# Kernel tuning notes

Hardware: AMD Instinct MI355X
Metric: run time of the kernel (lower is better)

Reference implementation:

```python
import jax, jax.numpy as jnp
import numpy as np

B, LQ, LKV = 4, 2048, 2048
E, AUG, H = 2048, 1024, 16
DH = E // H
EPS = 1e-6


def setup_inputs() -> dict:
    key = jax.random.key(0)
    ks = jax.random.split(key, 6)
    s = lambda d: 1.0 / np.sqrt(d)
    return {
        "query": jax.random.normal(ks[0], (B, LQ, E), jnp.float32),
        "aug_hidden_state": jax.random.normal(ks[1], (B, LKV, AUG), jnp.float32),
        "aug_mask": jnp.ones((B, LKV), jnp.float32),
        "proj_w": jax.random.normal(ks[2], (E, AUG), jnp.float32) * s(AUG),
        "proj_b": jnp.zeros((E,), jnp.float32),
        "in_proj_w": jax.random.normal(ks[3], (3 * E, E), jnp.float32) * s(E),
        "in_proj_b": jnp.zeros((3 * E,), jnp.float32),
        "out_proj_w": jax.random.normal(ks[4], (E, E), jnp.float32) * s(E),
        "out_proj_b": jnp.zeros((E,), jnp.float32),
        "rms_w": jnp.zeros((E,), jnp.float32),
    }


def reference(query, aug_hidden_state, aug_mask, proj_w, proj_b,
              in_proj_w, in_proj_b, out_proj_w, out_proj_b, rms_w):
    del aug_mask  # asserted but never used by the original forward
    # key and value: two identical Linear calls in the original -> same tensor
    kv = aug_hidden_state @ proj_w.T + proj_b                      # [B,LKV,E]
    wq, wk, wv = jnp.split(in_proj_w, 3, axis=0)
    bq, bk, bv = jnp.split(in_proj_b, 3, axis=0)
    q = (query @ wq.T + bq).reshape(B, LQ, H, DH)
    k = (kv @ wk.T + bk).reshape(B, LKV, H, DH)
    v = (kv @ wv.T + bv).reshape(B, LKV, H, DH)
    scale = 1.0 / np.sqrt(DH)
    scores = jnp.einsum("bqhd,bkhd->bhqk", q * scale, k)           # [B,H,LQ,LKV]
    attn = jax.nn.softmax(scores, axis=-1)
    ctx = jnp.einsum("bhqk,bkhd->bqhd", attn, v).reshape(B, LQ, E)
    attn_out = ctx @ out_proj_w.T + out_proj_b                      # [B,LQ,E]
    # GemmaRMSNorm: fp32 norm, (1 + weight) gain
    x32 = attn_out.astype(jnp.float32)
    normed = x32 * jax.lax.rsqrt(jnp.mean(x32 * x32, axis=-1, keepdims=True) + EPS)
    attn_out = (normed * (1.0 + rms_w)).astype(attn_out.dtype)
    return attn_out + query
```

## Files before the change

### kernel.cpp

```cpp
#include <hip/hip_runtime.h>
#include <hip/hip_bf16.h>
#include <stdint.h>

#define B_   4
#define LQ_  2048
#define LKV_ 2048
#define E_   2048
#define AUG_ 1024
#define H_   16
#define DH_  128

typedef unsigned short u16;
typedef __bf16 bf16x8 __attribute__((ext_vector_type(8)));
typedef float f32x4 __attribute__((ext_vector_type(4)));
typedef float f32x16 __attribute__((ext_vector_type(16)));
typedef int i32x2 __attribute__((ext_vector_type(2)));

__device__ __forceinline__ u16 f2bf(float f) {
  union { float f; unsigned u; } v; v.f = f;
  unsigned r = v.u + 0x7fffu + ((v.u >> 16) & 1u);
  return (u16)(r >> 16);
}
__device__ __forceinline__ unsigned pk2(float a, float b) {
  return (unsigned)f2bf(a) | ((unsigned)f2bf(b) << 16);
}
__device__ __forceinline__ float bf2f(u16 u) {
  union { unsigned u; float f; } v; v.u = (unsigned)u << 16; return v.f;
}
__device__ __forceinline__ unsigned cvtpk_bf16(float lo, float hi) {
  unsigned r;
  asm("v_cvt_pk_bf16_f32 %0, %1, %2" : "=v"(r) : "v"(lo), "v"(hi));
  return r;
}
__device__ __forceinline__ float fast_ex2(float x) {
  float r;
  asm("v_exp_f32 %0, %1" : "=v"(r) : "v"(x));
  return r;
}

#define GLDS(gsrc, ldst)                                                        \
  __builtin_amdgcn_global_load_lds(                                             \
      (__attribute__((address_space(1))) void*)(uintptr_t)(gsrc),               \
      (__attribute__((address_space(3))) void*)(unsigned)(uintptr_t)(ldst),     \
      16, 0, 0)

#define BARRIER()                                   \
  do {                                              \
    asm volatile("" ::: "memory");                  \
    __builtin_amdgcn_s_barrier();                   \
    asm volatile("" ::: "memory");                  \
  } while (0)

__global__ __launch_bounds__(256) void cast5(const float* __restrict__ p0, u16* __restrict__ o0, int c0,
                                             const float* __restrict__ p1, u16* __restrict__ o1, int c1,
                                             const float* __restrict__ p2, u16* __restrict__ o2, int c2,
                                             const float* __restrict__ p3, u16* __restrict__ o3, int c3,
                                             const float* __restrict__ p4, u16* __restrict__ o4, int c4) {
  int stride = gridDim.x * blockDim.x;
  for (int i = blockIdx.x * blockDim.x + threadIdx.x; i < c4; i += stride) {
    const float* in; u16* out; int j;
    if (i < c0)      { in = p0; out = o0; j = i; }
    else if (i < c1) { in = p1; out = o1; j = i - c0; }
    else if (i < c2) { in = p2; out = o2; j = i - c1; }
    else if (i < c3) { in = p3; out = o3; j = i - c2; }
    else             { in = p4; out = o4; j = i - c3; }
    const float4* p = (const float4*)in + (size_t)j * 2;
    float4 a = p[0], b = p[1];
    uint4 o;
    o.x = pk2(a.x, a.y); o.y = pk2(a.z, a.w);
    o.z = pk2(b.x, b.y); o.w = pk2(b.z, b.w);
    ((uint4*)out)[j] = o;
  }
}

template <int OUTF32>
__global__ __launch_bounds__(512, 2) void gemm_bt2(const u16* __restrict__ A,
                                                   const u16* __restrict__ W,
                                                   const float* __restrict__ bias,
                                                   void* __restrict__ Cp,
                                                   int N, int K) {
  __shared__ __align__(16) u16 As[3][256 * 32];
  __shared__ __align__(16) u16 Bs[3][256 * 32];
  const int tid = threadIdx.x;
  const int wave = tid >> 6, lane = tid & 63;
  const int wr = wave >> 2, wc = wave & 3;
  const int g = lane >> 4, r16 = lane & 15;
  const int m0 = blockIdx.y << 8, n0 = blockIdx.x << 8;

  size_t gA[2], gB[2];
  int ldst[2];
#pragma unroll
  for (int i = 0; i < 2; ++i) {
    int c = tid + i * 512;
    int s = c >> 6, w = c & 63;
    int wp = w ^ (((w >> 5) & 1) << 1);
    int grow = s * 16 + (wp >> 2);
    int gcol = (wp & 3) * 8;
    gA[i] = (size_t)(m0 + grow) * K + gcol;
    gB[i] = (size_t)(n0 + grow) * K + gcol;
    ldst[i] = c * 8;
  }
  const int aoff = r16 * 32 + ((g * 8) ^ ((r16 & 8) ? 16 : 0));

  f32x4 acc[8][4];
#pragma unroll
  for (int m = 0; m < 8; ++m)
#pragma unroll
    for (int n = 0; n < 4; ++n) acc[m][n] = (f32x4){0.f, 0.f, 0.f, 0.f};

  const int NT = K >> 5;
#pragma unroll
  for (int i = 0; i < 2; ++i) GLDS(A + gA[i], &As[0][ldst[i]]);
#pragma unroll
  for (int i = 0; i < 2; ++i) GLDS(W + gB[i], &Bs[0][ldst[i]]);
#pragma unroll
  for (int i = 0; i < 2; ++i) GLDS(A + gA[i] + 32, &As[1][ldst[i]]);
#pragma unroll
  for (int i = 0; i < 2; ++i) GLDS(W + gB[i] + 32, &Bs[1][ldst[i]]);

  int cur = 0;
  for (int t = 0; t < NT; ++t) {
    if (t + 1 < NT)
      asm volatile("s_waitcnt vmcnt(4)" ::: "memory");
    else
      asm volatile("s_waitcnt vmcnt(0)" ::: "memory");
    BARRIER();

    const u16* as = As[cur];
    const u16* bs = Bs[cur];
    int nxt = cur + 2; if (nxt >= 3) nxt -= 3;

    bf16x8 bfr[4], af[4];
#pragma unroll
    for (int n = 0; n < 4; ++n)
      bfr[n] = *(const bf16x8*)&bs[wc * 2048 + n * 512 + aoff];
#pragma unroll
    for (int m = 0; m < 4; ++m)
      af[m] = *(const bf16x8*)&as[wr * 4096 + m * 512 + aoff];
    if (t + 2 < NT) {
      size_t k0 = (size_t)(t + 2) * 32;
#pragma unroll
      for (int i = 0; i < 2; ++i) GLDS(A + gA[i] + k0, &As[nxt][ldst[i]]);
    }
    BARRIER();
    __builtin_amdgcn_s_setprio(1);
#pragma unroll
    for (int m = 0; m < 4; ++m)
#pragma unroll
      for (int n = 0; n < 4; ++n)
        acc[m][n] = __builtin_amdgcn_mfma_f32_16x16x32_bf16(af[m], bfr[n], acc[m][n], 0, 0, 0);
    __builtin_amdgcn_s_setprio(0);

    bf16x8 af2[4];
#pragma unroll
    for (int m = 0; m < 4; ++m)
      af2[m] = *(const bf16x8*)&as[wr * 4096 + (m + 4) * 512 + aoff];
    if (t + 2 < NT) {
      size_t k0 = (size_t)(t + 2) * 32;
#pragma unroll
      for (int i = 0; i < 2; ++i) GLDS(W + gB[i] + k0, &Bs[nxt][ldst[i]]);
    }
    BARRIER();
    __builtin_amdgcn_s_setprio(1);
#pragma unroll
    for (int m = 0; m < 4; ++m)
#pragma unroll
      for (int n = 0; n < 4; ++n)
        acc[m + 4][n] = __builtin_amdgcn_mfma_f32_16x16x32_bf16(af2[m], bfr[n], acc[m + 4][n], 0, 0, 0);
    __builtin_amdgcn_s_setprio(0);

    cur = cur + 1; if (cur >= 3) cur -= 3;
  }

  float bv[4];
#pragma unroll
  for (int n = 0; n < 4; ++n)
    bv[n] = bias ? bias[n0 + wc * 64 + n * 16 + r16] : 0.f;
#pragma unroll
  for (int m = 0; m < 8; ++m) {
    int row = m0 + wr * 128 + m * 16 + g * 4;
#pragma unroll
    for (int n = 0; n < 4; ++n) {
      int col = n0 + wc * 64 + n * 16 + r16;
#pragma unroll
      for (int r = 0; r < 4; ++r) {
        float v = acc[m][n][r] + bv[n];
        if (OUTF32)
          ((float*)Cp)[(size_t)(row + r) * N + col] = v;
        else
          ((u16*)Cp)[(size_t)(row + r) * N + col] = f2bf(v);
      }
    }
  }
}

__global__ __launch_bounds__(256) void transpose_v(const u16* __restrict__ v,
                                                   u16* __restrict__ vt) {
  __shared__ __align__(16) u16 t[64][72];
  int tid = threadIdx.x;
  int bh = blockIdx.z, b = bh >> 4, h = bh & 15;
  int kv0 = blockIdx.x << 6, d0 = blockIdx.y << 6;
  int gr = tid & 7, rw = tid >> 3;
#pragma unroll
  for (int p = 0; p < 2; ++p) {
    int row = rw + p * 32;
    uint4 x = *(const uint4*)&v[((size_t)(b * LKV_) + kv0 + row) * E_ + h * DH_ + d0 + gr * 8];
    *(uint4*)&t[row][gr * 8] = x;
  }
  __syncthreads();
#pragma unroll
  for (int p = 0; p < 2; ++p) {
    int d = rw + p * 32;
    u16 tmp[8];
#pragma unroll
    for (int j = 0; j < 8; ++j) tmp[j] = t[gr * 8 + j][d];
    uint4 o;
    o.x = (unsigned)tmp[0] | ((unsigned)tmp[1] << 16);
    o.y = (unsigned)tmp[2] | ((unsigned)tmp[3] << 16);
    o.z = (unsigned)tmp[4] | ((unsigned)tmp[5] << 16);
    o.w = (unsigned)tmp[6] | ((unsigned)tmp[7] << 16);
    *(uint4*)&vt[(((size_t)(b * H_ + h)) * DH_ + d0 + d) * LKV_ + kv0 + gr * 8] = o;
  }
}

__global__ __launch_bounds__(256) void attn_kernel(const u16* __restrict__ Q,
                                                   const u16* __restrict__ K,
                                                   const u16* __restrict__ Vt,
                                                   u16* __restrict__ Octx) {
  __shared__ __align__(16) u16 Ks[2][64 * 128];
  __shared__ __align__(16) u16 Vs[2][128 * 64];
  const int tid = threadIdx.x, wave = tid >> 6, lane = tid & 63;
  const int bid = blockIdx.x;
  const int qb = bid & 15, bh = bid >> 4, b = bh >> 4, h = bh & 15;
  const int q0 = qb << 7;
  const int l31 = lane & 31, hi = lane >> 5;
  const float Cs = 0.08838834764831845f * 1.4426950408889634f;

  const u16* Qp = Q + ((size_t)(b * LQ_ + q0 + wave * 32 + l31)) * E_ + h * DH_;
  const u16* Kp = K + ((size_t)(b * LKV_)) * E_ + h * DH_;
  const u16* Vp = Vt + (size_t)bh * DH_ * LKV_;

  const int kl_row = lane >> 4, kl_g = lane & 15;
  const int vl_row = lane >> 3, vl_g = lane & 7;

  bf16x8 qf[8];
#pragma unroll
  for (int c = 0; c < 8; ++c) {
    bf16x8 raw = *(const bf16x8*)&Qp[c * 16 + hi * 8];
#pragma unroll
    for (int j = 0; j < 8; ++j) qf[c][j] = (__bf16)((float)raw[j] * Cs);
  }

  bf16x8 VONES;
#pragma unroll
  for (int j = 0; j < 8; ++j) VONES[j] = (__bf16)1.0f;
  f32x16 FZERO = {};

  f32x16 o[4];
#pragma unroll
  for (int d = 0; d < 4; ++d)
#pragma unroll
    for (int r = 0; r < 16; ++r) o[d][r] = 0.f;
  f32x16 ol = {};

  auto STAGE = [&](int kv0, int buf) {
#pragma unroll
    for (int j = 0; j < 4; ++j) {
      int cc = wave * 4 + j;
      int krow = cc * 4 + kl_row;
      GLDS(Kp + (size_t)(kv0 + krow) * E_ + ((kl_g ^ (krow & 15)) << 3), &Ks[buf][cc * 512]);
      int vrow = cc * 8 + vl_row;
      GLDS(Vp + (size_t)vrow * LKV_ + kv0 + ((vl_g ^ (vrow & 7)) << 3), &Vs[buf][cc * 512]);
    }
  };

  const int NT = LKV_ / 64;
  STAGE(0, 0);

  for (int t = 0; t < NT; ++t) {
    const int cur = t & 1;
    if (t + 1 < NT) {
      STAGE((t + 1) * 64, cur ^ 1);
      asm volatile("s_waitcnt vmcnt(8)" ::: "memory");
    } else {
      asm volatile("s_waitcnt vmcnt(0)" ::: "memory");
    }
    BARRIER();

    const u16* ks = Ks[cur];
    const u16* vs = Vs[cur];

    f32x16 st[2];
#pragma unroll
    for (int n = 0; n < 2; ++n) {
      int row = n * 32 + l31;
      bf16x8 kf = *(const bf16x8*)&ks[row * 128 + ((hi ^ (row & 15)) << 3)];
      st[n] = __builtin_amdgcn_mfma_f32_32x32x16_bf16(kf, qf[0], FZERO, 0, 0, 0);
    }
#pragma unroll
    for (int c = 1; c < 8; ++c) {
#pragma unroll
      for (int n = 0; n < 2; ++n) {
        int row = n * 32 + l31;
        bf16x8 kf = *(const bf16x8*)&ks[row * 128 + (((c * 2 + hi) ^ (row & 15)) << 3)];
        st[n] = __builtin_amdgcn_mfma_f32_32x32x16_bf16(kf, qf[c], st[n], 0, 0, 0);
      }
    }

    unsigned AF[4][4];
#pragma unroll
    for (int n = 0; n < 2; ++n) {
      float pv[16];
#pragma unroll
      for (int r = 0; r < 16; ++r) pv[r] = fast_ex2(st[n][r]);
      unsigned a0 = cvtpk_bf16(pv[0], pv[1]),   a1 = cvtpk_bf16(pv[2], pv[3]);
      unsigned a2 = cvtpk_bf16(pv[4], pv[5]),   a3 = cvtpk_bf16(pv[6], pv[7]);
      unsigned b0 = cvtpk_bf16(pv[8], pv[9]),   b1 = cvtpk_bf16(pv[10], pv[11]);
      unsigned b2 = cvtpk_bf16(pv[12], pv[13]), b3 = cvtpk_bf16(pv[14], pv[15]);
      i32x2 r02 = __builtin_amdgcn_permlane32_swap((int)a0, (int)a2, false, false);
      i32x2 r13 = __builtin_amdgcn_permlane32_swap((int)a1, (int)a3, false, false);
      AF[n * 2][0] = (unsigned)r02[0]; AF[n * 2][1] = (unsigned)r13[0];
      AF[n * 2][2] = (unsigned)r02[1]; AF[n * 2][3] = (unsigned)r13[1];
      i32x2 s02 = __builtin_amdgcn_permlane32_swap((int)b0, (int)b2, false, false);
      i32x2 s13 = __builtin_amdgcn_permlane32_swap((int)b1, (int)b3, false, false);
      AF[n * 2 + 1][0] = (unsigned)s02[0]; AF[n * 2 + 1][1] = (unsigned)s13[0];
      AF[n * 2 + 1][2] = (unsigned)s02[1]; AF[n * 2 + 1][3] = (unsigned)s13[1];
    }

#pragma unroll
    for (int s = 0; s < 4; ++s) {
      union { unsigned u[4]; bf16x8 v; } pk;
      pk.u[0] = AF[s][0]; pk.u[1] = AF[s][1]; pk.u[2] = AF[s][2]; pk.u[3] = AF[s][3];
      bf16x8 pa = pk.v;
#pragma unroll
      for (int db = 0; db < 4; ++db) {
        int d = db * 32 + l31;
        bf16x8 vf = *(const bf16x8*)&vs[d * 64 + (((s * 2 + hi) ^ (d & 7)) << 3)];
        o[db] = __builtin_amdgcn_mfma_f32_32x32x16_bf16(pa, vf, o[db], 0, 0, 0);
      }
      ol = __builtin_amdgcn_mfma_f32_32x32x16_bf16(pa, VONES, ol, 0, 0, 0);
    }
    BARRIER();
  }

#pragma unroll
  for (int r = 0; r < 16; ++r) {
    int crow = (r & 3) + 8 * (r >> 2) + 4 * hi;
    float li = 1.0f / ol[r];
    size_t rb = ((size_t)(b * LQ_ + q0 + wave * 32 + crow)) * E_ + h * DH_ + l31;
#pragma unroll
    for (int db = 0; db < 4; ++db)
      Octx[rb + db * 32] = f2bf(o[db][r] * li);
  }
}

__global__ __launch_bounds__(256) void rms_res_bf(const u16* __restrict__ x,
                                                  const float* __restrict__ w,
                                                  const float* __restrict__ qres,
                                                  float* __restrict__ out) {
  int row = blockIdx.x, tid = threadIdx.x;
  uint4 xv = ((const uint4*)(x + (size_t)row * E_))[tid];
  float xf[8];
  xf[0] = bf2f((u16)(xv.x & 0xffff)); xf[1] = bf2f((u16)(xv.x >> 16));
  xf[2] = bf2f((u16)(xv.y & 0xffff)); xf[3] = bf2f((u16)(xv.y >> 16));
  xf[4] = bf2f((u16)(xv.z & 0xffff)); xf[5] = bf2f((u16)(xv.z >> 16));
  xf[6] = bf2f((u16)(xv.w & 0xffff)); xf[7] = bf2f((u16)(xv.w >> 16));
  float ss = 0.f;
#pragma unroll
  for (int j = 0; j < 8; ++j) ss += xf[j] * xf[j];
  ss += __shfl_xor(ss, 1);  ss += __shfl_xor(ss, 2);
  ss += __shfl_xor(ss, 4);  ss += __shfl_xor(ss, 8);
  ss += __shfl_xor(ss, 16); ss += __shfl_xor(ss, 32);
  __shared__ float ls[4];
  if ((tid & 63) == 0) ls[tid >> 6] = ss;
  __syncthreads();
  float total = ls[0] + ls[1] + ls[2] + ls[3];
  float rs = rsqrtf(total * (1.0f / (float)E_) + 1e-6f);
  const float4* qr = (const float4*)(qres + (size_t)row * E_);
  const float4* wr4 = (const float4*)w;
  float4 q0 = qr[tid * 2], q1 = qr[tid * 2 + 1];
  float4 w0 = wr4[tid * 2], w1 = wr4[tid * 2 + 1];
  float4 o0, o1;
  o0.x = xf[0] * rs * (1.f + w0.x) + q0.x;
  o0.y = xf[1] * rs * (1.f + w0.y) + q0.y;
  o0.z = xf[2] * rs * (1.f + w0.z) + q0.z;
  o0.w = xf[3] * rs * (1.f + w0.w) + q0.w;
  o1.x = xf[4] * rs * (1.f + w1.x) + q1.x;
  o1.y = xf[5] * rs * (1.f + w1.y) + q1.y;
  o1.z = xf[6] * rs * (1.f + w1.z) + q1.z;
  o1.w = xf[7] * rs * (1.f + w1.w) + q1.w;
  float4* op = (float4*)(out + (size_t)row * E_);
  op[tid * 2] = o0;
  op[tid * 2 + 1] = o1;
}

extern "C" void kernel_launch(void* const* d_in, const int* in_sizes, int n_in,
                              void* d_out, int out_size, void* d_ws, size_t ws_size,
                              hipStream_t stream) {
  const float* query = (const float*)d_in[0];
  const float* aug   = (const float*)d_in[1];
  const float* projw = (const float*)d_in[3];
  const float* projb = (const float*)d_in[4];
  const float* ipw   = (const float*)d_in[5];
  const float* ipb   = (const float*)d_in[6];
  const float* opw   = (const float*)d_in[7];
  const float* opb   = (const float*)d_in[8];
  const float* rmsw  = (const float*)d_in[9];

  char* ws = (char*)d_ws;
  size_t off = 0;
  auto alloc = [&](size_t bytes) {
    void* p = ws + off;
    off += (bytes + 1023) & ~(size_t)1023;
    return p;
  };
  u16* query_bf = (u16*)alloc((size_t)B_ * LQ_ * E_ * 2);
  u16* aug_bf   = (u16*)alloc((size_t)B_ * LKV_ * AUG_ * 2);
  u16* projw_bf = (u16*)alloc((size_t)E_ * AUG_ * 2);
  u16* w_bf     = (u16*)alloc((size_t)3 * E_ * E_ * 2);
  u16* outw_bf  = (u16*)alloc((size_t)E_ * E_ * 2);
  u16* kv_bf    = (u16*)alloc((size_t)B_ * LKV_ * E_ * 2);
  u16* q_bf     = (u16*)alloc((size_t)B_ * LQ_ * E_ * 2);
  u16* k_bf     = (u16*)alloc((size_t)B_ * LKV_ * E_ * 2);
  u16* v_bf     = (u16*)alloc((size_t)B_ * LKV_ * E_ * 2);
  u16* ctx_bf   = (u16*)alloc((size_t)B_ * LQ_ * E_ * 2);
  u16* attn_out = query_bf;
  u16* vt_bf = kv_bf;
  (void)in_sizes; (void)n_in; (void)ws_size;

  const int M = B_ * LQ_;

  const int n8_q  = (int)((size_t)M * E_ / 8);
  const int n8_a  = (int)((size_t)M * AUG_ / 8);
  const int n8_pw = (int)((size_t)E_ * AUG_ / 8);
  const int n8_iw = (int)((size_t)3 * E_ * E_ / 8);
  const int n8_ow = (int)((size_t)E_ * E_ / 8);
  const int cc0 = n8_q, cc1 = cc0 + n8_a, cc2 = cc1 + n8_pw, cc3 = cc2 + n8_iw,
            cc4 = cc3 + n8_ow;
  cast5<<<2048, 256, 0, stream>>>(query, query_bf, cc0,
                                  aug, aug_bf, cc1,
                                  projw, projw_bf, cc2,
                                  ipw, w_bf, cc3,
                                  opw, outw_bf, cc4);

  gemm_bt2<0><<<dim3(E_ / 256, M / 256), 512, 0, stream>>>(aug_bf, projw_bf, projb, kv_bf, E_, AUG_);
  gemm_bt2<0><<<dim3(E_ / 256, M / 256), 512, 0, stream>>>(query_bf, w_bf, ipb, q_bf, E_, E_);
  gemm_bt2<0><<<dim3(E_ / 256, M / 256), 512, 0, stream>>>(kv_bf, w_bf + (size_t)E_ * E_, ipb + E_, k_bf, E_, E_);
  gemm_bt2<0><<<dim3(E_ / 256, M / 256), 512, 0, stream>>>(kv_bf, w_bf + (size_t)2 * E_ * E_, ipb + 2 * E_, v_bf, E_, E_);
  transpose_v<<<dim3(LKV_ / 64, DH_ / 64, B_ * H_), 256, 0, stream>>>(v_bf, vt_bf);
  attn_kernel<<<B_ * H_ * (LQ_ / 128), 256, 0, stream>>>(q_bf, k_bf, vt_bf, ctx_bf);
  gemm_bt2<0><<<dim3(E_ / 256, M / 256), 512, 0, stream>>>(ctx_bf, outw_bf, opb, attn_out, E_, E_);
  rms_res_bf<<<M, 256, 0, stream>>>(attn_out, rmsw, query, (float*)d_out);
}
```

Before: 533.3 us.

## Software-pipeline attention QK/PV across tiles and trim GEMM barriers

The attention loop is restructured so that each iteration computes QK^T for tile t while doing the PV product for tile t-1. This lets the exp and pack work overlap with MFMA issue instead of serialising behind it. V gets a third LDS buffer so the pending PV tile is not overwritten by the prefetch, which raises LDS use per block. The projection GEMM main loop replaces two mid-iteration barriers with a single barrier at the end of the iteration, relying on the triple-buffered staging to keep it safe.

```diff
diff --git a/kernel.cpp b/kernel.cpp
--- a/kernel.cpp
+++ b/kernel.cpp
@@ -142,7 +142,6 @@
 #pragma unroll
       for (int i = 0; i < 2; ++i) GLDS(A + gA[i] + k0, &As[nxt][ldst[i]]);
     }
-    BARRIER();
     __builtin_amdgcn_s_setprio(1);
 #pragma unroll
     for (int m = 0; m < 4; ++m)
@@ -160,7 +159,6 @@
 #pragma unroll
       for (int i = 0; i < 2; ++i) GLDS(W + gB[i] + k0, &Bs[nxt][ldst[i]]);
     }
-    BARRIER();
     __builtin_amdgcn_s_setprio(1);
 #pragma unroll
     for (int m = 0; m < 4; ++m)
@@ -168,6 +166,7 @@
       for (int n = 0; n < 4; ++n)
         acc[m + 4][n] = __builtin_amdgcn_mfma_f32_16x16x32_bf16(af2[m], bfr[n], acc[m + 4][n], 0, 0, 0);
     __builtin_amdgcn_s_setprio(0);
+    BARRIER();
 
     cur = cur + 1; if (cur >= 3) cur -= 3;
   }
@@ -228,7 +227,7 @@
                                                    const u16* __restrict__ Vt,
                                                    u16* __restrict__ Octx) {
   __shared__ __align__(16) u16 Ks[2][64 * 128];
-  __shared__ __align__(16) u16 Vs[2][128 * 64];
+  __shared__ __align__(16) u16 Vs[3][128 * 64];
   const int tid = threadIdx.x, wave = tid >> 6, lane = tid & 63;
   const int bid = blockIdx.x;
   const int qb = bid & 15, bh = bid >> 4, b = bh >> 4, h = bh & 15;
@@ -263,34 +262,23 @@
     for (int r = 0; r < 16; ++r) o[d][r] = 0.f;
   f32x16 ol = {};
 
-  auto STAGE = [&](int kv0, int buf) {
+  auto STAGE_K = [&](int kv0, int buf) {
 #pragma unroll
     for (int j = 0; j < 4; ++j) {
       int cc = wave * 4 + j;
       int krow = cc * 4 + kl_row;
       GLDS(Kp + (size_t)(kv0 + krow) * E_ + ((kl_g ^ (krow & 15)) << 3), &Ks[buf][cc * 512]);
+    }
+  };
+  auto STAGE_V = [&](int kv0, int buf) {
+#pragma unroll
+    for (int j = 0; j < 4; ++j) {
+      int cc = wave * 4 + j;
       int vrow = cc * 8 + vl_row;
       GLDS(Vp + (size_t)vrow * LKV_ + kv0 + ((vl_g ^ (vrow & 7)) << 3), &Vs[buf][cc * 512]);
     }
   };
-
-  const int NT = LKV_ / 64;
-  STAGE(0, 0);
-
-  for (int t = 0; t < NT; ++t) {
-    const int cur = t & 1;
-    if (t + 1 < NT) {
-      STAGE((t + 1) * 64, cur ^ 1);
-      asm volatile("s_waitcnt vmcnt(8)" ::: "memory");
-    } else {
-      asm volatile("s_waitcnt vmcnt(0)" ::: "memory");
-    }
-    BARRIER();
-
-    const u16* ks = Ks[cur];
-    const u16* vs = Vs[cur];
-
-    f32x16 st[2];
+  auto QK = [&](const u16* ks, f32x16 st[2]) {
 #pragma unroll
     for (int n = 0; n < 2; ++n) {
       int row = n * 32 + l31;
@@ -306,8 +294,8 @@
         st[n] = __builtin_amdgcn_mfma_f32_32x32x16_bf16(kf, qf[c], st[n], 0, 0, 0);
       }
     }
-
-    unsigned AF[4][4];
+  };
+  auto PACK = [&](const f32x16 st[2], unsigned AF[4][4]) {
 #pragma unroll
     for (int n = 0; n < 2; ++n) {
       float pv[16];
@@ -326,7 +314,8 @@
       AF[n * 2 + 1][0] = (unsigned)s02[0]; AF[n * 2 + 1][1] = (unsigned)s13[0];
       AF[n * 2 + 1][2] = (unsigned)s02[1]; AF[n * 2 + 1][3] = (unsigned)s13[1];
     }
-
+  };
+  auto PV = [&](const unsigned AF[4][4], const u16* vs) {
 #pragma unroll
     for (int s = 0; s < 4; ++s) {
       union { unsigned u[4]; bf16x8 v; } pk;
@@ -340,8 +329,39 @@
       }
       ol = __builtin_amdgcn_mfma_f32_32x32x16_bf16(pa, VONES, ol, 0, 0, 0);
     }
-    BARRIER();
-  }
+  };
+
+  const int NT = LKV_ / 64;
+  STAGE_K(0, 0); STAGE_V(0, 0);
+  unsigned AFp[4][4];
+
+  {
+    STAGE_K(64, 1); STAGE_V(64, 1);
+    asm volatile("s_waitcnt vmcnt(8)" ::: "memory");
+    BARRIER();
+    f32x16 st[2];
+    QK(Ks[0], st);
+    PACK(st, AFp);
+    BARRIER();
+  }
+
+  for (int t = 1; t < NT; ++t) {
+    if (t + 1 < NT) {
+      STAGE_K((t + 1) * 64, (t + 1) & 1);
+      STAGE_V((t + 1) * 64, (t + 1) % 3);
+      asm volatile("s_waitcnt vmcnt(8)" ::: "memory");
+    } else {
+      asm volatile("s_waitcnt vmcnt(0)" ::: "memory");
+    }
+    BARRIER();
+
+    f32x16 st[2];
+    QK(Ks[t & 1], st);
+    PV(AFp, Vs[(t - 1) % 3]);
+    PACK(st, AFp);
+    BARRIER();
+  }
+  PV(AFp, Vs[(NT - 1) % 3]);
 
 #pragma unroll
   for (int r = 0; r < 16; ++r) {
```

New measurement: 529.0 us. No clear change (-0.8%).
